# Performance work log

Measured on AMD Instinct MI355X. Metric: run time of the kernel, lower is better.

The kernel has to match this reference:

```python
import jax, jax.numpy as jnp
import numpy as np

N_NODES = 50000
N_EDGES = 800000
EMB = 128
NUM_RADIAL = 6
CUTOFF = 5.0
ENV_EXP = 5
NUM_ATOM_TYPES = 95


def envelope(x):
    # DimeNet smooth cutoff envelope, p = exponent + 1
    p = ENV_EXP + 1
    a = -(p + 1) * (p + 2) / 2.0
    b = p * (p + 2)
    c = -p * (p + 1) / 2.0
    return 1.0 / x + a * x ** (p - 1) + b * x ** p + c * x ** (p + 1)


def setup_inputs() -> dict:
    key = jax.random.key(0)
    ks = jax.random.split(key, 10)
    Z = jax.random.randint(ks[0], (N_NODES,), 0, NUM_ATOM_TYPES)
    src = jax.random.randint(ks[1], (N_EDGES,), 0, N_NODES)
    dst = jax.random.randint(ks[2], (N_EDGES,), 0, N_NODES)
    rbf = jax.random.normal(ks[3], (N_EDGES, NUM_RADIAL), dtype=jnp.float32)
    # distances strictly inside (0, cutoff] to keep 1/x and sin(x)/x finite
    d = jax.random.uniform(ks[4], (N_EDGES,), dtype=jnp.float32,
                           minval=0.1, maxval=CUTOFF)
    emb_table = jax.random.uniform(ks[5], (NUM_ATOM_TYPES, EMB), dtype=jnp.float32,
                                   minval=-np.sqrt(3), maxval=np.sqrt(3))
    W_rbf = jax.random.normal(ks[6], (EMB, NUM_RADIAL), dtype=jnp.float32) * 0.3
    b_rbf = jnp.zeros((EMB,), dtype=jnp.float32)
    W_dense = jax.random.normal(ks[7], (EMB, 3 * EMB), dtype=jnp.float32) * 0.05
    b_dense = jnp.zeros((EMB,), dtype=jnp.float32)
    return {"Z": Z, "src": src, "dst": dst, "rbf": rbf, "d": d,
            "emb_table": emb_table, "W_rbf": W_rbf, "b_rbf": b_rbf,
            "W_dense": W_dense, "b_dense": b_dense}


def reference(Z, src, dst, rbf, d, emb_table, W_rbf, b_rbf, W_dense, b_dense):
    # node embedding: g.ndata['feat'] = embedding(Z)
    feat = emb_table[Z]                                  # [N, emb]
    # rbf projection + swish activation
    rbf_p = jax.nn.silu(rbf @ W_rbf.T + b_rbf)           # [E, emb]
    # gather src/dst node features, concat, dense, swish
    m = jnp.concatenate([feat[src], feat[dst], rbf_p], axis=-1)  # [E, 3*emb]
    m = jax.nn.silu(m @ W_dense.T + b_dense)             # [E, emb]
    # envelope * stacked bessel basis on scaled distances
    x = d / CUTOFF                                       # [E]
    n = jnp.arange(1, NUM_RADIAL + 1, dtype=jnp.float32)
    bessel = jnp.sin(n[None, :] * jnp.pi * x[:, None]) / x[:, None]  # [E, num_radial]
    rbf_env = envelope(x)[:, None] * bessel              # [E, num_radial]
    return m, rbf_env
```

## Files before the change

kernel.cpp:

```cpp
#include <hip/hip_runtime.h>
#include <hip/hip_bf16.h>

typedef _Float16 half8 __attribute__((ext_vector_type(8)));
typedef _Float16 half4 __attribute__((ext_vector_type(4)));
typedef float f32x4 __attribute__((ext_vector_type(4)));

#define E_TOTAL 800000
#define EMBD 128
#define KDIM 384
#define BM 64
#define APAD 392
#define WROW 40
#define SLAB_HALFS (128 * WROW)
#define NSLAB 12

__global__ __launch_bounds__(256) void prep_w(const float* __restrict__ Wd,
                                              _Float16* __restrict__ wsW) {
    int id = blockIdx.x * 256 + threadIdx.x;
    int c = id / KDIM;
    int k = id - c * KDIM;
    wsW[(k >> 5) * SLAB_HALFS + c * WROW + (k & 31)] = (_Float16)Wd[id];
}

__global__ __launch_bounds__(256) void env_kernel(const float* __restrict__ d,
                                                  float* __restrict__ out1) {
    int e = blockIdx.x * 256 + threadIdx.x;
    float x = d[e] * 0.2f;
    float inv = 1.0f / x;
    float x2 = x * x;
    float x5 = x2 * x2 * x;
    float env = inv + x5 * (-28.0f + x * (48.0f - 21.0f * x));
    float einv = env * inv;
    const float PI = 3.14159265358979323846f;
    float px = PI * x;
    float* o = out1 + e * 6;
    #pragma unroll
    for (int n = 1; n <= 6; n++) {
        o[n - 1] = einv * __sinf(px * (float)n);
    }
}

__global__ __launch_bounds__(256) void main_kernel(
    const int* __restrict__ Z, const int* __restrict__ src, const int* __restrict__ dst,
    const float* __restrict__ rbf, const float* __restrict__ emb,
    const float* __restrict__ W_rbf, const float* __restrict__ b_rbf,
    const float* __restrict__ b_dense, const _Float16* __restrict__ wsW,
    float* __restrict__ out0) {
    __shared__ _Float16 Alds[BM * APAD];
    __shared__ _Float16 Wlds[2 * SLAB_HALFS];
    __shared__ float s_wrbf[EMBD * 6];
    __shared__ float s_brbf[EMBD];
    __shared__ float s_bd[EMBD];

    const int tid = threadIdx.x;
    const int w = tid >> 6;
    const int l = tid & 63;
    const int e0 = blockIdx.x * BM;

    if (tid < EMBD) { s_brbf[tid] = b_rbf[tid]; s_bd[tid] = b_dense[tid]; }
    for (int i = tid; i < EMBD * 6; i += 256) s_wrbf[i] = W_rbf[i];

    {
        const float4* sv = (const float4*)(wsW);
        float4* dv = (float4*)(Wlds);
        for (int o = tid; o < 640; o += 256) dv[o] = sv[o];
    }
    __syncthreads();

    {
        int m = tid >> 2, q = tid & 3;
        int e = e0 + m;
        int zs = Z[src[e]];
        int zd = Z[dst[e]];
        const float4* rs = (const float4*)(emb + zs * EMBD) + q * 8;
        const float4* rd = (const float4*)(emb + zd * EMBD) + q * 8;
        _Float16* arow = &Alds[m * APAD];
        #pragma unroll
        for (int i = 0; i < 8; i++) {
            float4 f = rs[i];
            half4 h = {(_Float16)f.x, (_Float16)f.y, (_Float16)f.z, (_Float16)f.w};
            *(half4*)&arow[q * 32 + 4 * i] = h;
        }
        #pragma unroll
        for (int i = 0; i < 8; i++) {
            float4 f = rd[i];
            half4 h = {(_Float16)f.x, (_Float16)f.y, (_Float16)f.z, (_Float16)f.w};
            *(half4*)&arow[EMBD + q * 32 + 4 * i] = h;
        }
        const float* rb = rbf + e * 6;
        float r0 = rb[0], r1 = rb[1], r2 = rb[2], r3 = rb[3], r4 = rb[4], r5 = rb[5];
        for (int c0 = 0; c0 < 32; c0++) {
            int c = q * 32 + c0;
            const float* wr = &s_wrbf[c * 6];
            float pre = s_brbf[c] + r0 * wr[0] + r1 * wr[1] + r2 * wr[2] +
                        r3 * wr[3] + r4 * wr[4] + r5 * wr[5];
            float svl = pre / (1.0f + __expf(-pre));
            arow[2 * EMBD + c] = (_Float16)svl;
        }
    }
    __syncthreads();

    f32x4 acc[8];
    #pragma unroll
    for (int i = 0; i < 8; i++) acc[i] = (f32x4){0.f, 0.f, 0.f, 0.f};

    const int lr = l & 15;
    const int lg = l >> 4;

    #pragma unroll 2
    for (int s = 0; s < NSLAB; s++) {
        if (s < NSLAB - 1) {
            const float4* sv = (const float4*)(wsW + (s + 1) * SLAB_HALFS);
            float4* dv = (float4*)(Wlds + ((s + 1) & 1) * SLAB_HALFS);
            for (int o = tid; o < 640; o += 256) dv[o] = sv[o];
        }
        half8 a = *(const half8*)&Alds[(16 * w + lr) * APAD + 32 * s + lg * 8];
        const _Float16* wb = &Wlds[(s & 1) * SLAB_HALFS + lg * 8];
        #pragma unroll
        for (int nt = 0; nt < 8; nt++) {
            half8 b = *(const half8*)&wb[(nt * 16 + lr) * WROW];
            acc[nt] = __builtin_amdgcn_mfma_f32_16x16x32_f16(a, b, acc[nt], 0, 0, 0);
        }
        __syncthreads();
    }

    const int rowbase = e0 + 16 * w + lg * 4;
    #pragma unroll
    for (int nt = 0; nt < 8; nt++) {
        int col = nt * 16 + lr;
        float bd = s_bd[col];
        #pragma unroll
        for (int r = 0; r < 4; r++) {
            float v = acc[nt][r] + bd;
            v = v / (1.0f + __expf(-v));
            out0[(rowbase + r) * EMBD + col] = v;
        }
    }
}

extern "C" void kernel_launch(void* const* d_in, const int* in_sizes, int n_in,
                              void* d_out, int out_size, void* d_ws, size_t ws_size,
                              hipStream_t stream) {
    const int* Z = (const int*)d_in[0];
    const int* src = (const int*)d_in[1];
    const int* dst = (const int*)d_in[2];
    const float* rbf = (const float*)d_in[3];
    const float* dvec = (const float*)d_in[4];
    const float* emb = (const float*)d_in[5];
    const float* W_rbf = (const float*)d_in[6];
    const float* b_rbf = (const float*)d_in[7];
    const float* W_dense = (const float*)d_in[8];
    const float* b_dense = (const float*)d_in[9];

    float* out0 = (float*)d_out;
    float* out1 = out0 + (size_t)E_TOTAL * EMBD;
    _Float16* wsW = (_Float16*)d_ws;

    prep_w<<<(KDIM * EMBD) / 256, 256, 0, stream>>>(W_dense, wsW);
    env_kernel<<<E_TOTAL / 256, 256, 0, stream>>>(dvec, out1);
    main_kernel<<<E_TOTAL / BM, 256, 0, stream>>>(Z, src, dst, rbf, emb, W_rbf, b_rbf,
                                                  b_dense, wsW, out0);
}
```

Measured before the change: 801.0 us.

## Make main kernel persistent with resident LDS weights and register-fed MFMA operands

The dense kernel becomes persistent: 256 blocks of 512 threads each load the full fp16 weight matrix into LDS once. Each wave then loops over 32-edge tiles, building its A operands directly in registers from an fp16 copy of the embedding table and an in-register rbf projection. Index loads for the next tile are prefetched, and per-tile syncs and LDS staging of activations are removed. The env kernel now stages its output through LDS for coalesced float4 stores. In exchange, register pressure is higher and the grid is fixed, which may limit occupancy.

```diff
diff --git a/kernel.cpp b/kernel.cpp
--- a/kernel.cpp
+++ b/kernel.cpp
@@ -1,30 +1,37 @@
 #include <hip/hip_runtime.h>
-#include <hip/hip_bf16.h>
 
 typedef _Float16 half8 __attribute__((ext_vector_type(8)));
-typedef _Float16 half4 __attribute__((ext_vector_type(4)));
 typedef float f32x4 __attribute__((ext_vector_type(4)));
 
 #define E_TOTAL 800000
 #define EMBD 128
 #define KDIM 384
-#define BM 64
-#define APAD 392
-#define WROW 40
-#define SLAB_HALFS (128 * WROW)
 #define NSLAB 12
-
-__global__ __launch_bounds__(256) void prep_w(const float* __restrict__ Wd,
-                                              _Float16* __restrict__ wsW) {
+#define WSTRIDE 40
+#define SLAB_LDS (EMBD * WSTRIDE)
+#define WS_W_HALFS (KDIM * EMBD)
+#define N_TILES (E_TOTAL / 32)
+#define NBLOCKS 256
+#define NWAVES (NBLOCKS * 8)
+
+__global__ __launch_bounds__(256) void prep_kernel(const float* __restrict__ Wd,
+                                                   const float* __restrict__ emb,
+                                                   _Float16* __restrict__ ws) {
     int id = blockIdx.x * 256 + threadIdx.x;
-    int c = id / KDIM;
-    int k = id - c * KDIM;
-    wsW[(k >> 5) * SLAB_HALFS + c * WROW + (k & 31)] = (_Float16)Wd[id];
+    if (id < WS_W_HALFS) {
+        int n = id / KDIM, k = id - n * KDIM;
+        ws[(k >> 5) * (EMBD * 32) + n * 32 + (k & 31)] = (_Float16)Wd[id];
+    } else {
+        int j = id - WS_W_HALFS;
+        if (j < 95 * EMBD) ws[WS_W_HALFS + j] = (_Float16)emb[j];
+    }
 }
 
 __global__ __launch_bounds__(256) void env_kernel(const float* __restrict__ d,
                                                   float* __restrict__ out1) {
-    int e = blockIdx.x * 256 + threadIdx.x;
+    __shared__ float s[1536];
+    const int tid = threadIdx.x;
+    const int e = blockIdx.x * 256 + tid;
     float x = d[e] * 0.2f;
     float inv = 1.0f / x;
     float x2 = x * x;
@@ -33,107 +40,141 @@
     float einv = env * inv;
     const float PI = 3.14159265358979323846f;
     float px = PI * x;
-    float* o = out1 + e * 6;
     #pragma unroll
-    for (int n = 1; n <= 6; n++) {
-        o[n - 1] = einv * __sinf(px * (float)n);
-    }
-}
-
-__global__ __launch_bounds__(256) void main_kernel(
+    for (int n = 1; n <= 6; n++) s[tid * 6 + (n - 1)] = einv * __sinf(px * (float)n);
+    __syncthreads();
+    float4* ob = (float4*)(out1 + (size_t)blockIdx.x * 1536);
+    const float4* sv = (const float4*)s;
+    for (int k = tid; k < 384; k += 256) ob[k] = sv[k];
+}
+
+__global__ __launch_bounds__(512) void main_kernel(
     const int* __restrict__ Z, const int* __restrict__ src, const int* __restrict__ dst,
-    const float* __restrict__ rbf, const float* __restrict__ emb,
-    const float* __restrict__ W_rbf, const float* __restrict__ b_rbf,
-    const float* __restrict__ b_dense, const _Float16* __restrict__ wsW,
-    float* __restrict__ out0) {
-    __shared__ _Float16 Alds[BM * APAD];
-    __shared__ _Float16 Wlds[2 * SLAB_HALFS];
-    __shared__ float s_wrbf[EMBD * 6];
-    __shared__ float s_brbf[EMBD];
+    const float* __restrict__ rbf, const float* __restrict__ W_rbf,
+    const float* __restrict__ b_rbf, const float* __restrict__ b_dense,
+    const _Float16* __restrict__ ws, float* __restrict__ out0) {
+    __shared__ _Float16 Wlds[NSLAB * SLAB_LDS];
+    __shared__ float s_wrbfT[7 * EMBD];
     __shared__ float s_bd[EMBD];
 
     const int tid = threadIdx.x;
+
+    {
+        const half8* sv = (const half8*)ws;
+        for (int c = tid; c < 6144; c += 512) {
+            half8 v = sv[c];
+            int s = c >> 9, r = (c >> 2) & 127, q = c & 3;
+            *(half8*)&Wlds[s * SLAB_LDS + r * WSTRIDE + q * 8] = v;
+        }
+    }
+    for (int j = tid; j < 768; j += 512) {
+        int c = j / 6, i = j - c * 6;
+        s_wrbfT[i * EMBD + c] = W_rbf[j];
+    }
+    if (tid < EMBD) {
+        s_wrbfT[6 * EMBD + tid] = b_rbf[tid];
+        s_bd[tid] = b_dense[tid];
+    }
+    __syncthreads();
+
     const int w = tid >> 6;
     const int l = tid & 63;
-    const int e0 = blockIdx.x * BM;
-
-    if (tid < EMBD) { s_brbf[tid] = b_rbf[tid]; s_bd[tid] = b_dense[tid]; }
-    for (int i = tid; i < EMBD * 6; i += 256) s_wrbf[i] = W_rbf[i];
-
-    {
-        const float4* sv = (const float4*)(wsW);
-        float4* dv = (float4*)(Wlds);
-        for (int o = tid; o < 640; o += 256) dv[o] = sv[o];
-    }
-    __syncthreads();
-
-    {
-        int m = tid >> 2, q = tid & 3;
-        int e = e0 + m;
-        int zs = Z[src[e]];
-        int zd = Z[dst[e]];
-        const float4* rs = (const float4*)(emb + zs * EMBD) + q * 8;
-        const float4* rd = (const float4*)(emb + zd * EMBD) + q * 8;
-        _Float16* arow = &Alds[m * APAD];
-        #pragma unroll
-        for (int i = 0; i < 8; i++) {
-            float4 f = rs[i];
-            half4 h = {(_Float16)f.x, (_Float16)f.y, (_Float16)f.z, (_Float16)f.w};
-            *(half4*)&arow[q * 32 + 4 * i] = h;
-        }
-        #pragma unroll
-        for (int i = 0; i < 8; i++) {
-            float4 f = rd[i];
-            half4 h = {(_Float16)f.x, (_Float16)f.y, (_Float16)f.z, (_Float16)f.w};
-            *(half4*)&arow[EMBD + q * 32 + 4 * i] = h;
-        }
-        const float* rb = rbf + e * 6;
-        float r0 = rb[0], r1 = rb[1], r2 = rb[2], r3 = rb[3], r4 = rb[4], r5 = rb[5];
-        for (int c0 = 0; c0 < 32; c0++) {
-            int c = q * 32 + c0;
-            const float* wr = &s_wrbf[c * 6];
-            float pre = s_brbf[c] + r0 * wr[0] + r1 * wr[1] + r2 * wr[2] +
-                        r3 * wr[3] + r4 * wr[4] + r5 * wr[5];
-            float svl = pre / (1.0f + __expf(-pre));
-            arow[2 * EMBD + c] = (_Float16)svl;
-        }
-    }
-    __syncthreads();
-
-    f32x4 acc[8];
-    #pragma unroll
-    for (int i = 0; i < 8; i++) acc[i] = (f32x4){0.f, 0.f, 0.f, 0.f};
-
     const int lr = l & 15;
     const int lg = l >> 4;
-
-    #pragma unroll 2
-    for (int s = 0; s < NSLAB; s++) {
-        if (s < NSLAB - 1) {
-            const float4* sv = (const float4*)(wsW + (s + 1) * SLAB_HALFS);
-            float4* dv = (float4*)(Wlds + ((s + 1) & 1) * SLAB_HALFS);
-            for (int o = tid; o < 640; o += 256) dv[o] = sv[o];
-        }
-        half8 a = *(const half8*)&Alds[(16 * w + lr) * APAD + 32 * s + lg * 8];
-        const _Float16* wb = &Wlds[(s & 1) * SLAB_HALFS + lg * 8];
+    const int gw = blockIdx.x * 8 + w;
+
+    const half8* EB = (const half8*)(ws + WS_W_HALFS);
+
+    int t = gw;
+    int zsA, zdA, zsB, zdB;
+    {
+        int eA = t * 32 + lr;
+        int iA = src[eA], jA = dst[eA], iB = src[eA + 16], jB = dst[eA + 16];
+        zsA = Z[iA]; zdA = Z[jA]; zsB = Z[iB]; zdB = Z[jB];
+    }
+
+    for (; t < N_TILES; t += NWAVES) {
+        const int eA = t * 32 + lr;
+        half8 fa[12], fb[12];
+        #pragma unroll
+        for (int s4 = 0; s4 < 4; s4++) {
+            fa[s4]     = EB[zsA * 16 + s4 * 4 + lg];
+            fa[s4 + 4] = EB[zdA * 16 + s4 * 4 + lg];
+            fb[s4]     = EB[zsB * 16 + s4 * 4 + lg];
+            fb[s4 + 4] = EB[zdB * 16 + s4 * 4 + lg];
+        }
+        const float2* rpA = (const float2*)(rbf + (size_t)eA * 6);
+        const float2* rpB = (const float2*)(rbf + (size_t)(eA + 16) * 6);
+        float2 ra0 = rpA[0], ra1 = rpA[1], ra2 = rpA[2];
+        float2 rb0 = rpB[0], rb1 = rpB[1], rb2 = rpB[2];
+        float cra[6] = {ra0.x, ra0.y, ra1.x, ra1.y, ra2.x, ra2.y};
+        float crb[6] = {rb0.x, rb0.y, rb1.x, rb1.y, rb2.x, rb2.y};
+
+        const int t2 = t + NWAVES;
+        const bool more = (t2 < N_TILES);
+        int nsA = 0, ndA = 0, nsB = 0, ndB = 0;
+        if (more) {
+            int eA2 = t2 * 32 + lr;
+            nsA = src[eA2]; ndA = dst[eA2]; nsB = src[eA2 + 16]; ndB = dst[eA2 + 16];
+        }
+
+        #pragma unroll
+        for (int j4 = 0; j4 < 4; j4++) {
+            #pragma unroll
+            for (int jp = 0; jp < 4; jp++) {
+                const int c = 32 * j4 + lg * 8 + jp * 2;
+                float2 bb = *(const float2*)&s_wrbfT[6 * EMBD + c];
+                float pA0 = bb.x, pA1 = bb.y, pB0 = bb.x, pB1 = bb.y;
+                #pragma unroll
+                for (int i = 0; i < 6; i++) {
+                    float2 wv = *(const float2*)&s_wrbfT[i * EMBD + c];
+                    pA0 += cra[i] * wv.x; pA1 += cra[i] * wv.y;
+                    pB0 += crb[i] * wv.x; pB1 += crb[i] * wv.y;
+                }
+                pA0 *= __builtin_amdgcn_rcpf(1.0f + __expf(-pA0));
+                pA1 *= __builtin_amdgcn_rcpf(1.0f + __expf(-pA1));
+                pB0 *= __builtin_amdgcn_rcpf(1.0f + __expf(-pB0));
+                pB1 *= __builtin_amdgcn_rcpf(1.0f + __expf(-pB1));
+                fa[8 + j4][jp * 2]     = (_Float16)pA0;
+                fa[8 + j4][jp * 2 + 1] = (_Float16)pA1;
+                fb[8 + j4][jp * 2]     = (_Float16)pB0;
+                fb[8 + j4][jp * 2 + 1] = (_Float16)pB1;
+            }
+        }
+
+        if (more) { zsA = Z[nsA]; zdA = Z[ndA]; zsB = Z[nsB]; zdB = Z[ndB]; }
+
+        f32x4 acc0[8], acc1[8];
+        #pragma unroll
+        for (int i = 0; i < 8; i++) {
+            acc0[i] = (f32x4){0.f, 0.f, 0.f, 0.f};
+            acc1[i] = (f32x4){0.f, 0.f, 0.f, 0.f};
+        }
+        #pragma unroll
+        for (int s = 0; s < NSLAB; s++) {
+            const _Float16* wbase = &Wlds[s * SLAB_LDS + lg * 8];
+            #pragma unroll
+            for (int nt = 0; nt < 8; nt++) {
+                half8 b = *(const half8*)&wbase[(nt * 16 + lr) * WSTRIDE];
+                acc0[nt] = __builtin_amdgcn_mfma_f32_16x16x32_f16(fa[s], b, acc0[nt], 0, 0, 0);
+                acc1[nt] = __builtin_amdgcn_mfma_f32_16x16x32_f16(fb[s], b, acc1[nt], 0, 0, 0);
+            }
+        }
+
+        const int rbase = t * 32 + lg * 4;
         #pragma unroll
         for (int nt = 0; nt < 8; nt++) {
-            half8 b = *(const half8*)&wb[(nt * 16 + lr) * WROW];
-            acc[nt] = __builtin_amdgcn_mfma_f32_16x16x32_f16(a, b, acc[nt], 0, 0, 0);
-        }
-        __syncthreads();
-    }
-
-    const int rowbase = e0 + 16 * w + lg * 4;
-    #pragma unroll
-    for (int nt = 0; nt < 8; nt++) {
-        int col = nt * 16 + lr;
-        float bd = s_bd[col];
-        #pragma unroll
-        for (int r = 0; r < 4; r++) {
-            float v = acc[nt][r] + bd;
-            v = v / (1.0f + __expf(-v));
-            out0[(rowbase + r) * EMBD + col] = v;
+            const int col = nt * 16 + lr;
+            const float bd = s_bd[col];
+            #pragma unroll
+            for (int r = 0; r < 4; r++) {
+                float v = acc0[nt][r] + bd;
+                v *= __builtin_amdgcn_rcpf(1.0f + __expf(-v));
+                out0[(size_t)(rbase + r) * EMBD + col] = v;
+                float u = acc1[nt][r] + bd;
+                u *= __builtin_amdgcn_rcpf(1.0f + __expf(-u));
+                out0[(size_t)(rbase + 16 + r) * EMBD + col] = u;
+            }
         }
     }
 }
@@ -154,10 +195,10 @@
 
     float* out0 = (float*)d_out;
     float* out1 = out0 + (size_t)E_TOTAL * EMBD;
-    _Float16* wsW = (_Float16*)d_ws;
-
-    prep_w<<<(KDIM * EMBD) / 256, 256, 0, stream>>>(W_dense, wsW);
+    _Float16* wsH = (_Float16*)d_ws;
+
+    prep_kernel<<<240, 256, 0, stream>>>(W_dense, emb, wsH);
     env_kernel<<<E_TOTAL / 256, 256, 0, stream>>>(dvec, out1);
-    main_kernel<<<E_TOTAL / BM, 256, 0, stream>>>(Z, src, dst, rbf, emb, W_rbf, b_rbf,
-                                                  b_dense, wsW, out0);
-}
+    main_kernel<<<NBLOCKS, 512, 0, stream>>>(Z, src, dst, rbf, W_rbf, b_rbf, b_dense,
+                                             wsH, out0);
+}
```

New measurement: 1.198 ms. +49.6%, slower.
